# Kernel tuning notes

Measured on AMD Instinct MI355X. Metric: run time of the kernel, lower is better.

## Reference

```python
import jax, jax.numpy as jnp
import numpy as np

N, E, D = 100000, 1600000, 128

def setup_inputs() -> dict:
    key = jax.random.key(0)
    ks = jax.random.split(key, 6)
    x = jax.random.normal(ks[0], (N, D), dtype=jnp.float32)
    edge_index = jax.random.randint(ks[1], (2, E), 0, N, dtype=jnp.int64)
    edge_weight = jax.random.uniform(ks[2], (E, 1), dtype=jnp.float32)
    s = 1.0 / np.sqrt(D)  # glorot-ish scale
    W1 = jax.random.normal(ks[3], (D, D), dtype=jnp.float32) * s
    b1 = jnp.zeros((D,), dtype=jnp.float32)
    W2 = jax.random.normal(ks[4], (D, D), dtype=jnp.float32) * s
    b2 = jnp.zeros((D,), dtype=jnp.float32)
    return {"x": x, "edge_index": edge_index, "edge_weight": edge_weight,
            "W1": W1, "b1": b1, "W2": W2, "b2": b2}

def reference(x, edge_index, edge_weight, W1, b1, W2, b2):
    # wh_1 = w1(x)  -- computed in the original forward but unused (dead code)
    wh_1 = x @ W1 + b1
    # gather source-node features: [E, D]
    x_j = x[edge_index[0]]
    # edge_weight reshaped to [E, 1], elementwise scale
    ew = edge_weight.reshape(-1, 1)
    # scatter-sum into destination nodes: [N, D]
    agg = jax.ops.segment_sum(x_j * ew, edge_index[1], num_segments=x.shape[0])
    wh_2 = agg @ W2 + b2
    return wh_2
```

## Files before the change

kernel.cpp:

```cpp
#include <hip/hip_runtime.h>

#define D 128
#define BSH 9
#define BNODES 512
#define NBUK 256
#define CAP_B 9216
#define CAP_S 11264
#define EPB 8192

typedef __attribute__((ext_vector_type(4))) float f32x4;
typedef __attribute__((ext_vector_type(8))) short bf16x8;

__device__ __forceinline__ unsigned short f2bf(float f) {
    unsigned u = __float_as_uint(f);
    u += 0x7FFFu + ((u >> 16) & 1u);
    return (unsigned short)(u >> 16);
}
__device__ __forceinline__ unsigned pack2(float a, float b) {
    return (unsigned)f2bf(a) | ((unsigned)f2bf(b) << 16);
}
__device__ __forceinline__ float bflo(unsigned v) { return __uint_as_float(v << 16); }
__device__ __forceinline__ float bfhi(unsigned v) { return __uint_as_float(v & 0xFFFF0000u); }

__global__ __launch_bounds__(256) void cvtbin_kernel(
        const float4* __restrict__ x4, uint2* __restrict__ xb, int n4,
        const float* __restrict__ W2, unsigned short* __restrict__ w2b,
        const int* __restrict__ ei, const float* __restrict__ ew,
        int* __restrict__ bcur, uint2* __restrict__ brec, int E, int nbin) {
    __shared__ int lh[NBUK];
    __shared__ int lbase[NBUK];
    int t = threadIdx.x;

    if ((int)blockIdx.x < nbin) {
        int base0 = blockIdx.x * EPB;
        lh[t] = 0;
        __syncthreads();

        #pragma unroll 4
        for (int u = 0; u < EPB / 512; ++u) {
            int e = base0 + u * 512 + t * 2;
            if (e + 1 < E) {
                int2 d2 = *(const int2*)(ei + E + e);
                atomicAdd(&lh[d2.x >> BSH], 1);
                atomicAdd(&lh[d2.y >> BSH], 1);
            } else if (e < E) {
                atomicAdd(&lh[ei[E + e] >> BSH], 1);
            }
        }
        __syncthreads();
        lbase[t] = (lh[t] > 0) ? atomicAdd(&bcur[t], lh[t]) : 0;
        lh[t] = 0;
        __syncthreads();

        #pragma unroll 4
        for (int u = 0; u < EPB / 512; ++u) {
            int e = base0 + u * 512 + t * 2;
            if (e + 1 < E) {
                int2 s2 = *(const int2*)(ei + e);
                int2 d2 = *(const int2*)(ei + E + e);
                float2 w2 = *(const float2*)(ew + e);
                int b0 = d2.x >> BSH;
                int p0 = lbase[b0] + atomicAdd(&lh[b0], 1);
                if (p0 < CAP_B)
                    brec[(size_t)b0 * CAP_B + p0] = make_uint2(
                        ((unsigned)s2.x << BSH) | (unsigned)(d2.x & (BNODES - 1)),
                        __float_as_uint(w2.x));
                int b1 = d2.y >> BSH;
                int p1 = lbase[b1] + atomicAdd(&lh[b1], 1);
                if (p1 < CAP_B)
                    brec[(size_t)b1 * CAP_B + p1] = make_uint2(
                        ((unsigned)s2.y << BSH) | (unsigned)(d2.y & (BNODES - 1)),
                        __float_as_uint(w2.y));
            } else if (e < E) {
                int b0 = ei[E + e] >> BSH;
                int p0 = lbase[b0] + atomicAdd(&lh[b0], 1);
                if (p0 < CAP_B)
                    brec[(size_t)b0 * CAP_B + p0] = make_uint2(
                        ((unsigned)ei[e] << BSH) | (unsigned)(ei[E + e] & (BNODES - 1)),
                        __float_as_uint(ew[e]));
            }
        }
    } else {
        int bid = blockIdx.x - nbin;
        int nblk = gridDim.x - nbin;
        int tid = bid * 256 + t;
        int stride = nblk * 256;
        for (int i = tid; i < n4; i += stride) {
            float4 v = x4[i];
            xb[i] = make_uint2(pack2(v.x, v.y), pack2(v.z, v.w));
        }
        if (tid < D * D) {
            int j = tid >> 7, k = tid & 127;
            w2b[tid] = f2bf(W2[k * D + j]);
        }
    }
}

__global__ __launch_bounds__(256) void nodeify_kernel(
        const uint2* __restrict__ brec, const int* __restrict__ bcur,
        unsigned* __restrict__ srec, int2* __restrict__ offcnt, int N) {
    __shared__ int nh[BNODES];
    __shared__ int nb[BNODES];
    int b = blockIdx.x;
    int t = threadIdx.x;
    int cnt = bcur[b];
    if (cnt > CAP_B) cnt = CAP_B;
    const uint2* rec = brec + (size_t)b * CAP_B;

    nh[t] = 0; nh[t + 256] = 0;
    __syncthreads();
    for (int i = t; i < cnt; i += 256)
        atomicAdd(&nh[rec[i].x & (BNODES - 1)], 1);
    __syncthreads();

    int c0 = nh[2 * t], c1 = nh[2 * t + 1];
    int c0p = (c0 + 7) & ~7, c1p = (c1 + 7) & ~7;
    int run = c0p + c1p;
    nb[t] = run;
    __syncthreads();
    int val = run;
    for (int off = 1; off < 256; off <<= 1) {
        int other = (t >= off) ? nb[t - off] : 0;
        __syncthreads();
        val += other;
        nb[t] = val;
        __syncthreads();
    }
    int excl = val - run;
    __syncthreads();
    nb[2 * t] = excl;
    nb[2 * t + 1] = excl + c0p;

    int sbase = b * CAP_S;
    int node0 = b * BNODES;
    if (node0 + 2 * t < N)     offcnt[node0 + 2 * t]     = make_int2(sbase + excl,       c0p);
    if (node0 + 2 * t + 1 < N) offcnt[node0 + 2 * t + 1] = make_int2(sbase + excl + c0p, c1p);
    for (int p = c0; p < c0p; ++p) srec[(size_t)sbase + excl + p] = 0u;
    for (int p = c1; p < c1p; ++p) srec[(size_t)sbase + excl + c0p + p] = 0u;

    __syncthreads();
    nh[t] = 0; nh[t + 256] = 0;
    __syncthreads();

    for (int i = t; i < cnt; i += 256) {
        uint2 r = rec[i];
        int nl = r.x & (BNODES - 1);
        int rk = atomicAdd(&nh[nl], 1);
        unsigned src = r.x >> BSH;
        float w = __uint_as_float(r.y);
        int w15 = __float2int_rn(w * 32768.f);
        w15 = w15 < 0 ? 0 : (w15 > 32767 ? 32767 : w15);
        srec[(size_t)sbase + nb[nl] + rk] = (src << 15) | (unsigned)w15;
    }
}

__global__ __launch_bounds__(1024, 8) void gg_kernel(
        const unsigned* __restrict__ xb,
        const unsigned* __restrict__ srec,
        const int2* __restrict__ offcnt,
        const unsigned short* __restrict__ w2b,
        const float* __restrict__ b2,
        float* __restrict__ out, int N) {
    __shared__ unsigned At[16 * 66];
    int t = threadIdx.x, wave = t >> 6, lane = t & 63;
    int node0 = blockIdx.x * 16;
    int node = node0 + wave;

    int2 oc = offcnt[node];
    int beg = oc.x, total = oc.y;
    const char* xbase = (const char*)xb + lane * 4;
    float ax = 0.f, ay = 0.f;

    if (total <= 64) {
        unsigned rec = srec[beg + (lane < total ? lane : 0)];
        for (int r = 0; r + 8 <= total; r += 8) {
            unsigned q[8], v[8];
            #pragma unroll
            for (int u = 0; u < 8; ++u) q[u] = __shfl(rec, r + u);
            #pragma unroll
            for (int u = 0; u < 8; ++u)
                v[u] = *(const unsigned*)(xbase + ((q[u] & 0xFFFF8000u) >> 7));
            #pragma unroll
            for (int u = 0; u < 8; ++u) {
                float w = (float)(q[u] & 32767u);
                ax = fmaf(bflo(v[u]), w, ax);
                ay = fmaf(bfhi(v[u]), w, ay);
            }
        }
    } else {
        for (int j = beg; j < beg + total; ++j) {
            unsigned q0 = srec[j];
            unsigned v0 = *(const unsigned*)(xbase + ((q0 & 0xFFFF8000u) >> 7));
            float w0 = (float)(q0 & 32767u);
            ax = fmaf(bflo(v0), w0, ax);  ay = fmaf(bfhi(v0), w0, ay);
        }
    }
    At[wave * 66 + lane] = pack2(ax * (1.f / 32768.f), ay * (1.f / 32768.f));
    __syncthreads();

    if (wave < 8) {
        int r = lane & 15, g = lane >> 4;
        int col = wave * 16 + r;

        bf16x8 afr[4];
        #pragma unroll
        for (int kk = 0; kk < 4; ++kk)
            afr[kk] = *(const bf16x8*)((const char*)At + r * 264 + kk * 64 + g * 16);

        f32x4 acc = (f32x4){0.f, 0.f, 0.f, 0.f};
        #pragma unroll
        for (int kk = 0; kk < 4; ++kk) {
            bf16x8 bfr = *(const bf16x8*)(w2b + col * D + kk * 32 + g * 8);
            acc = __builtin_amdgcn_mfma_f32_16x16x32_bf16(afr[kk], bfr, acc, 0, 0, 0);
        }

        float bias = b2[col];
        float* o = out + (size_t)(node0 + g * 4) * D + col;
        o[0]     = acc[0] + bias;
        o[D]     = acc[1] + bias;
        o[2 * D] = acc[2] + bias;
        o[3 * D] = acc[3] + bias;
    }
}

extern "C" void kernel_launch(void* const* d_in, const int* in_sizes, int n_in,
                              void* d_out, int out_size, void* d_ws, size_t ws_size,
                              hipStream_t stream) {
    const float* x  = (const float*)d_in[0];
    const int*   ei = (const int*)d_in[1];
    const float* ew = (const float*)d_in[2];
    const float* W2 = (const float*)d_in[5];
    const float* b2 = (const float*)d_in[6];
    float* out = (float*)d_out;

    int N = in_sizes[0] / D;
    int E = in_sizes[2];

    int NB = (N + BNODES - 1) / BNODES;

    char* ws = (char*)d_ws;
    unsigned* xb   = (unsigned*)ws;
    unsigned* srec = (unsigned*)(ws + (size_t)N * 256);
    int2* offcnt   = (int2*)((char*)srec + (size_t)NB * CAP_S * 4);
    unsigned short* w2b = (unsigned short*)((char*)offcnt + (size_t)N * 8);
    int* bcur      = (int*)((char*)w2b + (size_t)D * D * 2);
    uint2* brec    = (uint2*)d_out;

    hipMemsetAsync(bcur, 0, NBUK * sizeof(int), stream);

    int nbin = (E + EPB - 1) / EPB;
    cvtbin_kernel<<<nbin + 1600, 256, 0, stream>>>(
        (const float4*)x, (uint2*)xb, N * D / 4, W2, w2b,
        ei, ew, bcur, brec, E, nbin);

    nodeify_kernel<<<NB, 256, 0, stream>>>(brec, bcur, srec, offcnt, N);

    gg_kernel<<<N / 16, 1024, 0, stream>>>(xb, srec, offcnt, w2b, b2, out, N);
}
```

Baseline: 136.7 us.

## Sort nodes by padded degree class so each gather block has balanced waves

Nodeify now builds a histogram of nodes by padded in-degree class. A new permfill kernel uses it to write a permutation that groups nodes in descending degree order. The gather/GEMM kernel reads node ids through this permutation, so the 16 waves in a block handle nodes of similar degree, which cuts intra-block imbalance and tail effects. The cost is an extra kernel launch, global atomics, an indirect node lookup, and scattered output-row writes.

```diff
diff --git a/kernel.cpp b/kernel.cpp
--- a/kernel.cpp
+++ b/kernel.cpp
@@ -7,6 +7,7 @@
 #define CAP_B 9216
 #define CAP_S 11264
 #define EPB 8192
+#define NCLS 13
 
 typedef __attribute__((ext_vector_type(4))) float f32x4;
 typedef __attribute__((ext_vector_type(8))) short bf16x8;
@@ -98,9 +99,11 @@
 
 __global__ __launch_bounds__(256) void nodeify_kernel(
         const uint2* __restrict__ brec, const int* __restrict__ bcur,
-        unsigned* __restrict__ srec, int2* __restrict__ offcnt, int N) {
+        unsigned* __restrict__ srec, int2* __restrict__ offcnt,
+        int* __restrict__ dcnt, int N) {
     __shared__ int nh[BNODES];
     __shared__ int nb[BNODES];
+    __shared__ int ch[NCLS];
     int b = blockIdx.x;
     int t = threadIdx.x;
     int cnt = bcur[b];
@@ -108,6 +111,7 @@
     const uint2* rec = brec + (size_t)b * CAP_B;
 
     nh[t] = 0; nh[t + 256] = 0;
+    if (t < NCLS) ch[t] = 0;
     __syncthreads();
     for (int i = t; i < cnt; i += 256)
         atomicAdd(&nh[rec[i].x & (BNODES - 1)], 1);
@@ -133,12 +137,22 @@
 
     int sbase = b * CAP_S;
     int node0 = b * BNODES;
-    if (node0 + 2 * t < N)     offcnt[node0 + 2 * t]     = make_int2(sbase + excl,       c0p);
-    if (node0 + 2 * t + 1 < N) offcnt[node0 + 2 * t + 1] = make_int2(sbase + excl + c0p, c1p);
+    if (node0 + 2 * t < N) {
+        offcnt[node0 + 2 * t] = make_int2(sbase + excl, c0p);
+        int cls = c0p >> 3; if (cls > NCLS - 1) cls = NCLS - 1;
+        atomicAdd(&ch[cls], 1);
+    }
+    if (node0 + 2 * t + 1 < N) {
+        offcnt[node0 + 2 * t + 1] = make_int2(sbase + excl + c0p, c1p);
+        int cls = c1p >> 3; if (cls > NCLS - 1) cls = NCLS - 1;
+        atomicAdd(&ch[cls], 1);
+    }
     for (int p = c0; p < c0p; ++p) srec[(size_t)sbase + excl + p] = 0u;
     for (int p = c1; p < c1p; ++p) srec[(size_t)sbase + excl + c0p + p] = 0u;
 
     __syncthreads();
+    if (t < NCLS && ch[t] > 0) atomicAdd(&dcnt[t], ch[t]);
+
     nh[t] = 0; nh[t + 256] = 0;
     __syncthreads();
 
@@ -154,17 +168,51 @@
     }
 }
 
+__global__ __launch_bounds__(256) void permfill_kernel(
+        const int2* __restrict__ offcnt, const int* __restrict__ dcnt,
+        int* __restrict__ dcur, int* __restrict__ perm, int N) {
+    __shared__ int base[NCLS];
+    __shared__ int lh[NCLS], lbase[NCLS];
+    int t = threadIdx.x;
+    if (t == 0) {
+        int s = 0;
+        for (int c = NCLS - 1; c >= 0; --c) { base[c] = s; s += dcnt[c]; }
+    }
+    if (t < NCLS) lh[t] = 0;
+    __syncthreads();
+
+    int node = blockIdx.x * 256 + t;
+    int cls = 0;
+    if (node < N) {
+        cls = offcnt[node].y >> 3; if (cls > NCLS - 1) cls = NCLS - 1;
+        atomicAdd(&lh[cls], 1);
+    }
+    __syncthreads();
+    if (t < NCLS) {
+        lbase[t] = lh[t] ? atomicAdd(&dcur[t], lh[t]) : 0;
+        lh[t] = 0;
+    }
+    __syncthreads();
+    if (node < N) {
+        int r = atomicAdd(&lh[cls], 1);
+        perm[base[cls] + lbase[cls] + r] = node;
+    }
+}
+
 __global__ __launch_bounds__(1024, 8) void gg_kernel(
         const unsigned* __restrict__ xb,
         const unsigned* __restrict__ srec,
         const int2* __restrict__ offcnt,
+        const int* __restrict__ perm,
         const unsigned short* __restrict__ w2b,
         const float* __restrict__ b2,
         float* __restrict__ out, int N) {
     __shared__ unsigned At[16 * 66];
+    __shared__ int nid[16];
     int t = threadIdx.x, wave = t >> 6, lane = t & 63;
-    int node0 = blockIdx.x * 16;
-    int node = node0 + wave;
+    int slot0 = blockIdx.x * 16;
+    int node = perm[slot0 + wave];
+    if (lane == 0) nid[wave] = node;
 
     int2 oc = offcnt[node];
     int beg = oc.x, total = oc.y;
@@ -215,11 +263,9 @@
         }
 
         float bias = b2[col];
-        float* o = out + (size_t)(node0 + g * 4) * D + col;
-        o[0]     = acc[0] + bias;
-        o[D]     = acc[1] + bias;
-        o[2 * D] = acc[2] + bias;
-        o[3 * D] = acc[3] + bias;
+        #pragma unroll
+        for (int i = 0; i < 4; ++i)
+            out[(size_t)nid[g * 4 + i] * D + col] = acc[i] + bias;
     }
 }
 
@@ -242,18 +288,23 @@
     unsigned* xb   = (unsigned*)ws;
     unsigned* srec = (unsigned*)(ws + (size_t)N * 256);
     int2* offcnt   = (int2*)((char*)srec + (size_t)NB * CAP_S * 4);
-    unsigned short* w2b = (unsigned short*)((char*)offcnt + (size_t)N * 8);
+    int* perm      = (int*)((char*)offcnt + (size_t)N * 8);
+    unsigned short* w2b = (unsigned short*)((char*)perm + (size_t)N * 4);
     int* bcur      = (int*)((char*)w2b + (size_t)D * D * 2);
+    int* dcnt      = bcur + NBUK;
+    int* dcur      = dcnt + NCLS;
     uint2* brec    = (uint2*)d_out;
 
-    hipMemsetAsync(bcur, 0, NBUK * sizeof(int), stream);
+    hipMemsetAsync(bcur, 0, (NBUK + 2 * NCLS) * sizeof(int), stream);
 
     int nbin = (E + EPB - 1) / EPB;
     cvtbin_kernel<<<nbin + 1600, 256, 0, stream>>>(
         (const float4*)x, (uint2*)xb, N * D / 4, W2, w2b,
         ei, ew, bcur, brec, E, nbin);
 
-    nodeify_kernel<<<NB, 256, 0, stream>>>(brec, bcur, srec, offcnt, N);
-
-    gg_kernel<<<N / 16, 1024, 0, stream>>>(xb, srec, offcnt, w2b, b2, out, N);
-}
+    nodeify_kernel<<<NB, 256, 0, stream>>>(brec, bcur, srec, offcnt, dcnt, N);
+
+    permfill_kernel<<<(N + 255) / 256, 256, 0, stream>>>(offcnt, dcnt, dcur, perm, N);
+
+    gg_kernel<<<N / 16, 1024, 0, stream>>>(xb, srec, offcnt, perm, w2b, b2, out, N);
+}
```

Result: slower. 149.0 us (+9.1%).
